# Optimization experiments

Measured on AMD Instinct MI355X. Metric: run time of the kernel, lower is better.

The kernel has to match this reference:

```python
import jax, jax.numpy as jnp
import numpy as np

N_HEADS = 4


def _fq_sym(x, qmax=127.0):
    # symmetric per-tensor dynamic int8 fake-quant with straight-through estimator
    scale = jnp.maximum(jnp.max(jnp.abs(x)) / qmax, 1e-8)
    q = jnp.clip(jnp.round(x / scale), -qmax, qmax) * scale
    return x + jax.lax.stop_gradient(q - x)


def _fq_unsigned(x, qmax=255.0):
    # unsigned 8-bit fake-quant (for softmax probabilities in [0,1])
    scale = jnp.maximum(jnp.max(x) / qmax, 1e-8)
    q = jnp.clip(jnp.round(x / scale), 0.0, qmax) * scale
    return x + jax.lax.stop_gradient(q - x)


def setup_inputs() -> dict:
    key = jax.random.key(0)
    kq, kk, kv = jax.random.split(key, 3)
    shape = (16, 256, 32, 32)  # [B, n_heads*head_dim, H, W]
    return {
        "q": jax.random.normal(kq, shape, dtype=jnp.float32),
        "k": jax.random.normal(kk, shape, dtype=jnp.float32),
        "v": jax.random.normal(kv, shape, dtype=jnp.float32),
    }


def reference(q, k, v):
    b, c, h, w = q.shape
    d = c // N_HEADS
    s = h * w

    def split_heads(x):
        # b (n d) h w -> b n (h w) d
        return jnp.swapaxes(x.reshape(b, N_HEADS, d, s), -1, -2)

    qh, kh, vh = split_heads(q), split_heads(k), split_heads(v)  # [b,n,s,d]
    scale = d ** (-0.5)

    # QuanMMHead: fake-quantize both operands, then matmul, scaled by 1/sqrt(d)
    attn = jnp.einsum("bnsd,bntd->bnst", _fq_sym(qh), _fq_sym(kh)) * scale
    # QuanSoftmax: softmax then fake-quantize probabilities
    attn = _fq_unsigned(jax.nn.softmax(attn, axis=-1))
    # QuanMMHead for attn @ V
    out = jnp.einsum("bnst,bntd->bnsd", _fq_sym(attn), _fq_sym(vh))  # [b,n,s,d]

    # b n s d -> b (n d) h w
    out = jnp.swapaxes(out, -1, -2).reshape(b, c, h, w)
    return out
```

## Files before the change

kernel.cpp:

```cpp
#include <hip/hip_runtime.h>
#include <math.h>

#define NBN 64
#define DD  64
#define SS  1024

typedef int i32x4_ __attribute__((ext_vector_type(4)));

#if defined(__has_builtin)
#  if __has_builtin(__builtin_amdgcn_exp2f)
#    define FEXP2(x) __builtin_amdgcn_exp2f(x)
#  endif
#endif
#ifndef FEXP2
#  define FEXP2(x) exp2f(x)
#endif

#if defined(__has_builtin)
#  if __has_builtin(__builtin_amdgcn_cvt_pk_u8_f32)
#    define PK_U8(f, r, old) __builtin_amdgcn_cvt_pk_u8_f32((f), (r), (old))
#  endif
#endif
#ifndef PK_U8
#  define PK_U8(f, r, old) (((old) & ~(0xff << (8*(r)))) | (((int)(f) & 0xff) << (8*(r))))
#endif

__device__ __forceinline__ i32x4_ mfma_i8(i32x4_ a, i32x4_ b, i32x4_ c) {
    return __builtin_amdgcn_mfma_i32_16x16x64_i8(a, b, c, 0, 0, 0);
}

__device__ __forceinline__ int quant_sym(float x, float sc) {
    float r = fminf(fmaxf(rintf(x / sc), -127.0f), 127.0f);
    return (int)r;
}

__device__ __forceinline__ float wave_max256(const float* part, int lane) {
    float4 t = ((const float4*)part)[lane];
    float m = fmaxf(fmaxf(t.x, t.y), fmaxf(t.z, t.w));
    #pragma unroll
    for (int mk = 1; mk <= 32; mk <<= 1) m = fmaxf(m, __shfl_xor(m, mk, 64));
    return m;
}

__device__ __forceinline__ float wave_min2048(const float* part, int lane) {
    float4 t = ((const float4*)part)[lane];
    float m = fminf(fminf(t.x, t.y), fminf(t.z, t.w));
    #pragma unroll
    for (int i = 1; i < 8; ++i) {
        float4 u = ((const float4*)part)[lane + i * 64];
        m = fminf(m, fminf(fminf(u.x, u.y), fminf(u.z, u.w)));
    }
    #pragma unroll
    for (int mk = 1; mk <= 32; mk <<= 1) m = fminf(m, __shfl_xor(m, mk, 64));
    return m;
}

__global__ void k_absmax(const float* __restrict__ q, const float* __restrict__ k,
                         const float* __restrict__ v, float* __restrict__ amax_part) {
    const float* src = (blockIdx.y == 0) ? q : (blockIdx.y == 1) ? k : v;
    const int n = NBN * DD * SS;
    float m = 0.0f;
    for (int i = (blockIdx.x * 256 + threadIdx.x) * 4; i < n; i += gridDim.x * 256 * 4) {
        float4 x = *(const float4*)(src + i);
        m = fmaxf(m, fmaxf(fmaxf(fabsf(x.x), fabsf(x.y)), fmaxf(fabsf(x.z), fabsf(x.w))));
    }
    __shared__ float red[256];
    red[threadIdx.x] = m;
    __syncthreads();
    for (int off = 128; off > 0; off >>= 1) {
        if (threadIdx.x < off) red[threadIdx.x] = fmaxf(red[threadIdx.x], red[threadIdx.x + off]);
        __syncthreads();
    }
    if (threadIdx.x == 0) amax_part[blockIdx.y * 256 + blockIdx.x] = red[0];
}

__global__ void k_quant_qkv(const float* __restrict__ q, const float* __restrict__ k,
                            const float* __restrict__ v, const float* __restrict__ amax_part,
                            int* __restrict__ Qp, int* __restrict__ Kp, int* __restrict__ Vq) {
    __shared__ float TlA[64][69];
    __shared__ __align__(16) int TlB[64][20];
    const int which = blockIdx.z;
    const int bn = blockIdx.y;
    const int tid = threadIdx.x;
    const float sc = fmaxf(wave_max256(amax_part + which * 256, tid & 63) / 127.0f, 1e-8f);
    if (which < 2) {
        const float* tsrc = (which ? k : q) + (size_t)bn * DD * SS;
        int* dst = which ? Kp : Qp;
        const int s_base = blockIdx.x * 64;
        #pragma unroll
        for (int kk = 0; kk < 4; ++kk) {
            int idx = tid + kk * 256;
            int d = idx >> 4, s4 = idx & 15;
            float4 x = *(const float4*)(tsrc + (size_t)d * SS + s_base + s4 * 4);
            TlA[d][s4*4+0] = x.x; TlA[d][s4*4+1] = x.y;
            TlA[d][s4*4+2] = x.z; TlA[d][s4*4+3] = x.w;
        }
        __syncthreads();
        const int u = tid & 3, s_loc = tid >> 2;
        int pw[4];
        #pragma unroll
        for (int jj = 0; jj < 4; ++jj) {
            int p = 0;
            #pragma unroll
            for (int r = 0; r < 4; ++r) {
                int iq = quant_sym(TlA[16*u + 4*jj + r][s_loc], sc);
                p |= (iq & 0xff) << (8 * r);
            }
            pw[jj] = p;
        }
        *(int4*)(dst + ((size_t)bn * SS + s_base + s_loc) * 16 + u * 4)
            = make_int4(pw[0], pw[1], pw[2], pw[3]);
    } else {
        const int tb = blockIdx.x;
        {
            const int d = tid >> 2, tqq = tid & 3;
            #pragma unroll
            for (int i = 0; i < 4; ++i) {
                const int tq = tqq * 4 + i;
                float4 x = *(const float4*)(v + (size_t)(bn * 64 + d) * SS + tb * 64 + tq * 4);
                TlB[d][tq] = (quant_sym(x.x, sc) & 0xff)
                          | ((quant_sym(x.y, sc) & 0xff) << 8)
                          | ((quant_sym(x.z, sc) & 0xff) << 16)
                          | ((quant_sym(x.w, sc) & 0xff) << 24);
            }
        }
        __syncthreads();
        {
            const int dt = tid >> 6, gg = (tid >> 4) & 3;
            const int d = dt * 16 + (tid & 15);
            int4 w = make_int4(TlB[d][gg*4+0], TlB[d][gg*4+1], TlB[d][gg*4+2], TlB[d][gg*4+3]);
            *(int4*)(Vq + (size_t)(bn * 16 + tb) * 1024 + tid * 4) = w;
        }
    }
}

__global__ __launch_bounds__(512) void k_phase_a(const int* __restrict__ Qp,
    const int* __restrict__ Kp, const float* __restrict__ amax_part,
    float* __restrict__ m2_arr, float* __restrict__ l_arr, float* __restrict__ minl_part)
{
    __shared__ float Mf[8][32];
    __shared__ float Lf[8][32];
    const int x = blockIdx.x;
    const int bn = ((x & 7) << 3) | ((x >> 3) & 7);
    const int s0 = blockIdx.y * 32;
    const int tid = threadIdx.x;
    const int wv = tid >> 6, lane = tid & 63;
    const int g = lane >> 4, c = lane & 15;
    const float aq = wave_max256(amax_part, lane);
    const float ak = wave_max256(amax_part + 256, lane);
    const float sq = fmaxf(aq / 127.0f, 1e-8f);
    const float sk = fmaxf(ak / 127.0f, 1e-8f);
    const float cqk2 = (sq * sk * 0.125f) * 1.4426950408889634f;
    const i32x4_ qf0 = *(const i32x4_*)(Qp + ((size_t)bn * SS + s0 + c) * 16 + g * 4);
    const i32x4_ qf1 = *(const i32x4_*)(Qp + ((size_t)bn * SS + s0 + 16 + c) * 16 + g * 4);
    const i32x4_ zero = {0, 0, 0, 0};
    const int* kb = Kp + ((size_t)bn * SS + wv * 128 + c) * 16 + g * 4;

    i32x4_ kfr[8];
    #pragma unroll
    for (int j = 0; j < 8; ++j) kfr[j] = *(const i32x4_*)(kb + j * 256);
    __builtin_amdgcn_sched_barrier(0);
    i32x4_ dq0[8], dq1[8];
    #pragma unroll
    for (int j = 0; j < 8; ++j) {
        dq0[j] = mfma_i8(kfr[j], qf0, zero);
        dq1[j] = mfma_i8(kfr[j], qf1, zero);
    }

    int im0 = -2147483647, im1 = -2147483647;
    #pragma unroll
    for (int j = 0; j < 8; ++j) {
        im0 = max(im0, max(max(dq0[j][0], dq0[j][1]), max(dq0[j][2], dq0[j][3])));
        im1 = max(im1, max(max(dq1[j][0], dq1[j][1]), max(dq1[j][2], dq1[j][3])));
    }
    im0 = max(im0, __shfl_xor(im0, 16, 64));
    im0 = max(im0, __shfl_xor(im0, 32, 64));
    im1 = max(im1, __shfl_xor(im1, 16, 64));
    im1 = max(im1, __shfl_xor(im1, 32, 64));
    const float m0 = (float)im0 * cqk2;
    const float m1 = (float)im1 * cqk2;
    float la0 = 0.0f, lb0 = 0.0f, lc0 = 0.0f, ld0 = 0.0f;
    float la1 = 0.0f, lb1 = 0.0f, lc1 = 0.0f, ld1 = 0.0f;
    #pragma unroll
    for (int j = 0; j < 8; ++j) {
        la0 += FEXP2(fmaf((float)dq0[j][0], cqk2, -m0));
        lb0 += FEXP2(fmaf((float)dq0[j][1], cqk2, -m0));
        lc0 += FEXP2(fmaf((float)dq0[j][2], cqk2, -m0));
        ld0 += FEXP2(fmaf((float)dq0[j][3], cqk2, -m0));
        la1 += FEXP2(fmaf((float)dq1[j][0], cqk2, -m1));
        lb1 += FEXP2(fmaf((float)dq1[j][1], cqk2, -m1));
        lc1 += FEXP2(fmaf((float)dq1[j][2], cqk2, -m1));
        ld1 += FEXP2(fmaf((float)dq1[j][3], cqk2, -m1));
    }
    float l0 = (la0 + lb0) + (lc0 + ld0);
    float l1 = (la1 + lb1) + (lc1 + ld1);
    l0 += __shfl_xor(l0, 16, 64);
    l0 += __shfl_xor(l0, 32, 64);
    l1 += __shfl_xor(l1, 16, 64);
    l1 += __shfl_xor(l1, 32, 64);
    if (g == 0) {
        Mf[wv][c] = m0;      Lf[wv][c] = l0;
        Mf[wv][16 + c] = m1; Lf[wv][16 + c] = l1;
    }
    __syncthreads();
    if (tid < 32) {
        const int cc = tid;
        float m = Mf[0][cc];
        #pragma unroll
        for (int w = 1; w < 8; ++w) m = fmaxf(m, Mf[w][cc]);
        float l = 0.0f;
        #pragma unroll
        for (int w = 0; w < 8; ++w) l += Lf[w][cc] * FEXP2(Mf[w][cc] - m);
        m2_arr[bn * SS + s0 + cc] = m;
        l_arr[bn * SS + s0 + cc] = l;
        float lm = l;
        #pragma unroll
        for (int mk = 1; mk <= 16; mk <<= 1) lm = fminf(lm, __shfl_xor(lm, mk, 64));
        if (cc == 0) minl_part[blockIdx.y * 64 + blockIdx.x] = lm;
    }
}

__global__ __launch_bounds__(512) void k_phase_b(const int* __restrict__ Qp,
    const int* __restrict__ Kp, const int* __restrict__ Vq,
    const float* __restrict__ amax_part, const float* __restrict__ minl_part,
    const float* __restrict__ m2_arr, const float* __restrict__ l_arr,
    float* __restrict__ out)
{
    __shared__ __align__(16) int Kst[2][2][1024];
    __shared__ __align__(16) int Vst[2][2][1024];
    __shared__ __align__(16) int PlS[2816];
    const int f = blockIdx.x + (blockIdx.y << 4);
    const int bn = ((f & 7) << 3) | ((f >> 3) & 7);
    const int sblk = (f >> 6) * 64;
    const int tid = threadIdx.x;
    const int wv = tid >> 6, lane = tid & 63;
    const int g = lane >> 4, c = lane & 15;
    const int sgrp = wv & 3, th = wv >> 2;
    const int s0 = sblk + sgrp * 16;
    const float sq = fmaxf(wave_max256(amax_part, lane) / 127.0f, 1e-8f);
    const float sk = fmaxf(wave_max256(amax_part + 256, lane) / 127.0f, 1e-8f);
    const float sv = fmaxf(wave_max256(amax_part + 512, lane) / 127.0f, 1e-8f);
    const float minl = wave_min2048(minl_part, lane);
    const float cqk2 = (sq * sk * 0.125f) * 1.4426950408889634f;
    const float maxP     = 1.0f / minl;
    const float scale_p  = fmaxf(maxP / 255.0f, 1e-8f);
    const float scale_p2 = fmaxf((255.0f * scale_p) / 127.0f, 1e-8f);
    const float cpv = scale_p2 * sv;
    const float m2 = m2_arr[bn * SS + s0 + c];
    const float l  = l_arr [bn * SS + s0 + c];
    const float bexp = log2f((1.0f / scale_p) / l) - m2;
    const i32x4_ qf = *(const i32x4_*)(Qp + ((size_t)bn * SS + s0 + c) * 16 + g * 4);
    const i32x4_ zero = {0, 0, 0, 0};
    int* myP = PlS + wv * 320;
    const int woff = c * 20 + g * 4;
    const int tb0 = th * 8;
    const int soff = sgrp * 256 + lane * 4;
    const int* kg = Kp + (size_t)bn * SS * 16 + soff;
    const int* vg = Vq + (size_t)bn * 16384 + soff;

    i32x4_ acc[4] = {zero, zero, zero, zero};

    {
        i32x4_ gk = *(const i32x4_*)(kg + tb0 * 1024);
        i32x4_ gv = *(const i32x4_*)(vg + tb0 * 1024);
        *(i32x4_*)&Kst[0][th][soff] = gk;
        *(i32x4_*)&Vst[0][th][soff] = gv;
    }
    __syncthreads();

    #pragma unroll
    for (int i = 0; i < 8; ++i) {
        const int b = i & 1;
        i32x4_ gk, gv;
        if (i < 7) {
            gk = *(const i32x4_*)(kg + (tb0 + i + 1) * 1024);
            gv = *(const i32x4_*)(vg + (tb0 + i + 1) * 1024);
        }
        __builtin_amdgcn_sched_barrier(0);
        int W[4];
        #pragma unroll
        for (int j = 0; j < 4; ++j) {
            i32x4_ kf = *(const i32x4_*)&Kst[b][th][j * 256 + c * 16 + g * 4];
            i32x4_ dq = mfma_i8(kf, qf, zero);
            int w = 0;
            #pragma unroll
            for (int r = 0; r < 4; ++r) {
                float xx = FEXP2(fmaf((float)dq[r], cqk2, bexp));
                w = PK_U8(rintf(xx), r, w);
            }
            W[j] = (w >> 1) & 0x7f7f7f7f;
        }
        i32x4_ wv4 = {W[0], W[1], W[2], W[3]};
        *(i32x4_*)(myP + woff) = wv4;
        i32x4_ pa;
        pa[0] = myP[c * 20 + 0 + g];
        pa[1] = myP[c * 20 + 4 + g];
        pa[2] = myP[c * 20 + 8 + g];
        pa[3] = myP[c * 20 + 12 + g];
        #pragma unroll
        for (int dt = 0; dt < 4; ++dt) {
            i32x4_ vf = *(const i32x4_*)&Vst[b][th][dt * 256 + g * 64 + c * 4];
            acc[dt] = mfma_i8(pa, vf, acc[dt]);
        }
        if (i < 7) {
            *(i32x4_*)&Kst[b ^ 1][th][soff] = gk;
            *(i32x4_*)&Vst[b ^ 1][th][soff] = gv;
        }
        __syncthreads();
    }

    int* sbuf = PlS;
    #pragma unroll
    for (int ch = 0; ch < 2; ++ch) {
        if (th == 0) {
            #pragma unroll
            for (int dt = 0; dt < 2; ++dt)
                #pragma unroll
                for (int r = 0; r < 4; ++r)
                    sbuf[(dt * 16 + c) * 67 + sgrp * 16 + 4 * g + r] = acc[ch * 2 + dt][r];
        }
        __syncthreads();
        if (th == 1) {
            #pragma unroll
            for (int dt = 0; dt < 2; ++dt)
                #pragma unroll
                for (int r = 0; r < 4; ++r) {
                    const int slot = (dt * 16 + c) * 67 + sgrp * 16 + 4 * g + r;
                    ((float*)sbuf)[slot] = (float)(sbuf[slot] + acc[ch * 2 + dt][r]) * cpv;
                }
        }
        __syncthreads();
        {
            const int d = tid >> 4, sq4 = tid & 15;
            const float* fb = (const float*)sbuf + d * 67 + sq4 * 4;
            float4 val = make_float4(fb[0], fb[1], fb[2], fb[3]);
            *(float4*)(out + (size_t)bn * 65536 + (size_t)(ch * 32 + d) * 1024 + sblk + sq4 * 4) = val;
        }
        __syncthreads();
    }
}

extern "C" void kernel_launch(void* const* d_in, const int* in_sizes, int n_in,
                              void* d_out, int out_size, void* d_ws, size_t ws_size,
                              hipStream_t stream) {
    const float* q = (const float*)d_in[0];
    const float* k = (const float*)d_in[1];
    const float* v = (const float*)d_in[2];
    float* out = (float*)d_out;
    char* ws = (char*)d_ws;

    float* amax_part = (float*)ws;
    float* minl_part = (float*)(ws + 4096);
    int* Qp      = (int*)(ws + 16384);
    int* Kp      = (int*)(ws + 16384 + (size_t)(1 << 22));
    int* Vq      = (int*)(ws + 16384 + (size_t)(2 << 22));
    float* m2    = (float*)(ws + 16384 + (size_t)(3 << 22));
    float* l_a   = (float*)(ws + 16384 + (size_t)(3 << 22) + (1 << 18));

    k_absmax<<<dim3(256, 3), 256, 0, stream>>>(q, k, v, amax_part);
    k_quant_qkv<<<dim3(16, NBN, 3), 256, 0, stream>>>(q, k, v, amax_part, Qp, Kp, Vq);
    k_phase_a<<<dim3(64, 32), 512, 0, stream>>>(Qp, Kp, amax_part, m2, l_a, minl_part);
    k_phase_b<<<dim3(16, NBN), 512, 0, stream>>>(Qp, Kp, Vq, amax_part, minl_part, m2, l_a, out);
}
```

Measured before the change: 66.14 us.

## Single-buffer K/V tiles in a pooled LDS region to raise phase-B occupancy

Replaces the double-buffered K/V shared-memory tiles and separate P buffer with one pooled LDS array. The K/V tiles become single-buffered, with an extra barrier before each overwrite. The epilogue reduction is done in one pass over all 64 d values, and launch bounds now request 8 blocks per CU. The goal is to cut LDS use per block so more blocks fit on a CU. The cost is an extra barrier per iteration and less overlap between global loads and compute.

```diff
diff --git a/kernel.cpp b/kernel.cpp
--- a/kernel.cpp
+++ b/kernel.cpp
@@ -220,15 +220,13 @@
     }
 }
 
-__global__ __launch_bounds__(512) void k_phase_b(const int* __restrict__ Qp,
+__global__ __launch_bounds__(512, 8) void k_phase_b(const int* __restrict__ Qp,
     const int* __restrict__ Kp, const int* __restrict__ Vq,
     const float* __restrict__ amax_part, const float* __restrict__ minl_part,
     const float* __restrict__ m2_arr, const float* __restrict__ l_arr,
     float* __restrict__ out)
 {
-    __shared__ __align__(16) int Kst[2][2][1024];
-    __shared__ __align__(16) int Vst[2][2][1024];
-    __shared__ __align__(16) int PlS[2816];
+    __shared__ __align__(16) int POOL[6912];
     const int f = blockIdx.x + (blockIdx.y << 4);
     const int bn = ((f & 7) << 3) | ((f >> 3) & 7);
     const int sblk = (f >> 6) * 64;
@@ -251,7 +249,9 @@
     const float bexp = log2f((1.0f / scale_p) / l) - m2;
     const i32x4_ qf = *(const i32x4_*)(Qp + ((size_t)bn * SS + s0 + c) * 16 + g * 4);
     const i32x4_ zero = {0, 0, 0, 0};
-    int* myP = PlS + wv * 320;
+    int* Kst = POOL + th * 1024;
+    int* Vst = POOL + 2048 + th * 1024;
+    int* myP = POOL + 4096 + wv * 320;
     const int woff = c * 20 + g * 4;
     const int tb0 = th * 8;
     const int soff = sgrp * 256 + lane * 4;
@@ -263,14 +263,13 @@
     {
         i32x4_ gk = *(const i32x4_*)(kg + tb0 * 1024);
         i32x4_ gv = *(const i32x4_*)(vg + tb0 * 1024);
-        *(i32x4_*)&Kst[0][th][soff] = gk;
-        *(i32x4_*)&Vst[0][th][soff] = gv;
+        *(i32x4_*)&Kst[soff] = gk;
+        *(i32x4_*)&Vst[soff] = gv;
     }
     __syncthreads();
 
     #pragma unroll
     for (int i = 0; i < 8; ++i) {
-        const int b = i & 1;
         i32x4_ gk, gv;
         if (i < 7) {
             gk = *(const i32x4_*)(kg + (tb0 + i + 1) * 1024);
@@ -280,7 +279,7 @@
         int W[4];
         #pragma unroll
         for (int j = 0; j < 4; ++j) {
-            i32x4_ kf = *(const i32x4_*)&Kst[b][th][j * 256 + c * 16 + g * 4];
+            i32x4_ kf = *(const i32x4_*)&Kst[j * 256 + c * 16 + g * 4];
             i32x4_ dq = mfma_i8(kf, qf, zero);
             int w = 0;
             #pragma unroll
@@ -299,44 +298,43 @@
         pa[3] = myP[c * 20 + 12 + g];
         #pragma unroll
         for (int dt = 0; dt < 4; ++dt) {
-            i32x4_ vf = *(const i32x4_*)&Vst[b][th][dt * 256 + g * 64 + c * 4];
+            i32x4_ vf = *(const i32x4_*)&Vst[dt * 256 + g * 64 + c * 4];
             acc[dt] = mfma_i8(pa, vf, acc[dt]);
         }
+        __syncthreads();
         if (i < 7) {
-            *(i32x4_*)&Kst[b ^ 1][th][soff] = gk;
-            *(i32x4_*)&Vst[b ^ 1][th][soff] = gv;
-        }
-        __syncthreads();
-    }
-
-    int* sbuf = PlS;
-    #pragma unroll
-    for (int ch = 0; ch < 2; ++ch) {
-        if (th == 0) {
-            #pragma unroll
-            for (int dt = 0; dt < 2; ++dt)
-                #pragma unroll
-                for (int r = 0; r < 4; ++r)
-                    sbuf[(dt * 16 + c) * 67 + sgrp * 16 + 4 * g + r] = acc[ch * 2 + dt][r];
-        }
-        __syncthreads();
-        if (th == 1) {
-            #pragma unroll
-            for (int dt = 0; dt < 2; ++dt)
-                #pragma unroll
-                for (int r = 0; r < 4; ++r) {
-                    const int slot = (dt * 16 + c) * 67 + sgrp * 16 + 4 * g + r;
-                    ((float*)sbuf)[slot] = (float)(sbuf[slot] + acc[ch * 2 + dt][r]) * cpv;
-                }
-        }
-        __syncthreads();
-        {
-            const int d = tid >> 4, sq4 = tid & 15;
-            const float* fb = (const float*)sbuf + d * 67 + sq4 * 4;
-            float4 val = make_float4(fb[0], fb[1], fb[2], fb[3]);
-            *(float4*)(out + (size_t)bn * 65536 + (size_t)(ch * 32 + d) * 1024 + sblk + sq4 * 4) = val;
-        }
-        __syncthreads();
+            *(i32x4_*)&Kst[soff] = gk;
+            *(i32x4_*)&Vst[soff] = gv;
+            __syncthreads();
+        }
+    }
+
+    int* sbuf = POOL;
+    if (th == 0) {
+        #pragma unroll
+        for (int dt = 0; dt < 4; ++dt)
+            #pragma unroll
+            for (int r = 0; r < 4; ++r)
+                sbuf[(dt * 16 + c) * 67 + sgrp * 16 + 4 * g + r] = acc[dt][r];
+    }
+    __syncthreads();
+    if (th == 1) {
+        #pragma unroll
+        for (int dt = 0; dt < 4; ++dt)
+            #pragma unroll
+            for (int r = 0; r < 4; ++r) {
+                const int slot = (dt * 16 + c) * 67 + sgrp * 16 + 4 * g + r;
+                ((float*)sbuf)[slot] = (float)(sbuf[slot] + acc[dt][r]) * cpv;
+            }
+    }
+    __syncthreads();
+    #pragma unroll
+    for (int u = 0; u < 2; ++u) {
+        const int chunk = tid + u * 512;
+        const int d = chunk >> 4, sq4 = chunk & 15;
+        const float* fb = (const float*)sbuf + d * 67 + sq4 * 4;
+        float4 val = make_float4(fb[0], fb[1], fb[2], fb[3]);
+        *(float4*)(out + (size_t)bn * 65536 + (size_t)d * 1024 + sblk + sq4 * 4) = val;
     }
 }
 
```

Result: no change. 66.80 us (+1.0%).
